# Kernel optimization log

Hardware: AMD Instinct MI355X
Metric: run time of the kernel (lower is better)

The kernel has to match this reference:

```python
import math
import jax, jax.numpy as jnp
import numpy as np

B, FEAT, H, W = 4, 256, 48, 48
NH = 8
PE = 10            # pe_dim -> 3*PE = 30 positional channels
DK = FEAT // NH    # 32
DV = FEAT // NH    # 32
SCALE = 2.0 * math.pi
TEMPERATURE = 10000.0
BN_EPS = 1e-5


def pos_en_sine(h, w, num_pos_feats=PE):
    """3-axis sine positional encoding (y, x, and a constant 'o' axis) -> [3*PE, h, w]."""
    eps = 1e-6
    ones = jnp.ones((h, w), jnp.float32)
    y_embed = jnp.cumsum(ones, axis=0)
    x_embed = jnp.cumsum(ones, axis=1)
    y_embed = y_embed / (y_embed[-1:, :] + eps) * SCALE
    x_embed = x_embed / (x_embed[:, -1:] + eps) * SCALE
    o_embed = ones * SCALE  # third axis, constant when no explicit pos is given
    dim_t = jnp.arange(num_pos_feats, dtype=jnp.float32)
    dim_t = TEMPERATURE ** (2.0 * jnp.floor(dim_t / 2.0) / num_pos_feats)

    def enc(e):  # e: [h, w] -> [h, w, PE] interleaved sin/cos
        p = e[..., None] / dim_t
        return jnp.stack([jnp.sin(p[..., 0::2]), jnp.cos(p[..., 1::2])], axis=-1).reshape(h, w, num_pos_feats)

    pe = jnp.concatenate([enc(y_embed), enc(x_embed), enc(o_embed)], axis=-1)  # [h, w, 3*PE]
    return jnp.transpose(pe, (2, 0, 1))  # [3*PE, h, w]


def conv1x1(w, x):  # w: [out_c, in_c], x: [b, in_c, h, w]
    return jnp.einsum('oc,bchw->bohw', w, x)


def setup_inputs() -> dict:
    key = jax.random.key(0)
    ks = jax.random.split(key, 16)
    s = 0.02
    return {
        'q': jax.random.normal(ks[0], (B, FEAT, H, W), jnp.float32),
        'k': jax.random.normal(ks[1], (B, FEAT, H, W), jnp.float32),
        'v': jax.random.normal(ks[2], (B, FEAT, H, W), jnp.float32),
        'wq': jax.random.normal(ks[3], (NH * DK, FEAT + 3 * PE), jnp.float32) * s,
        'wk': jax.random.normal(ks[4], (NH * DK, FEAT + 3 * PE), jnp.float32) * s,
        'wv': jax.random.normal(ks[5], (NH * DV, FEAT), jnp.float32) * s,
        'wfc': jax.random.normal(ks[6], (FEAT, NH * DV), jnp.float32) * s,
        'w1': jax.random.normal(ks[7], (FEAT, FEAT), jnp.float32) * s,
        'b1': jnp.zeros((FEAT,), jnp.float32),
        'w2': jax.random.normal(ks[8], (FEAT, FEAT), jnp.float32) * s,
        'b2': jnp.zeros((FEAT,), jnp.float32),
        'gamma': jnp.ones((FEAT,), jnp.float32),
        'beta': jnp.zeros((FEAT,), jnp.float32),
    }


def reference(q, k, v, wq, wk, wv, wfc, w1, b1, w2, b2, gamma, beta):
    b, c, h, w = q.shape
    n = h * w
    pe = pos_en_sine(h, w)                                # [3*PE, h, w]
    peb = jnp.broadcast_to(pe[None], (b,) + pe.shape)
    qc = jnp.concatenate([q, peb], axis=1)                # [b, FEAT+30, h, w]
    kc = jnp.concatenate([k, peb], axis=1)
    # multi-head softmax attention over all spatial tokens
    Q = conv1x1(wq, qc).reshape(b, NH, DK, n)             # [b, nh, dk, n]
    K = conv1x1(wk, kc).reshape(b, NH, DK, n)
    V = conv1x1(wv, v).reshape(b, NH, DV, n)
    scores = jnp.einsum('bhdn,bhdm->bhnm', Q, K) / jnp.sqrt(jnp.float32(DK))
    attn = jax.nn.softmax(scores, axis=-1)                # [b, nh, n, n]
    O = jnp.einsum('bhnm,bhdm->bhdn', attn, V).reshape(b, NH * DV, h, w)
    O = conv1x1(wfc, O)                                   # [b, FEAT, h, w]
    # pointwise FFN + residual
    h1 = jax.nn.relu(conv1x1(w1, O) + b1[None, :, None, None])
    h2 = conv1x1(w2, h1) + b2[None, :, None, None]
    out = O + h2
    # BatchNorm2d (training mode: batch statistics over (b, h, w), biased var)
    mean = jnp.mean(out, axis=(0, 2, 3), keepdims=True)
    var = jnp.var(out, axis=(0, 2, 3), keepdims=True)
    out = (out - mean) / jnp.sqrt(var + BN_EPS)
    out = out * gamma[None, :, None, None] + beta[None, :, None, None]
    return out
```

## Files before the change

### kernel.cpp

```cpp
#include <hip/hip_runtime.h>
#include <hip/hip_bf16.h>

#define NTOK 2304

typedef short  short8  __attribute__((ext_vector_type(8)));
typedef unsigned short ushort8v __attribute__((ext_vector_type(8)));
typedef float  f32x4   __attribute__((ext_vector_type(4)));

static __device__ __forceinline__ unsigned short f2bfu(float f){
  __hip_bfloat16 h = __float2bfloat16(f);
  union { __hip_bfloat16 h; unsigned short u; } cv; cv.h = h; return cv.u;
}

static __device__ __forceinline__ void plane32(unsigned &a, unsigned &b){
  asm("v_permlane32_swap_b32 %0, %1" : "+v"(a), "+v"(b));
}
static __device__ __forceinline__ void plane16(unsigned &a, unsigned &b){
  asm("v_permlane16_swap_b32 %0, %1" : "+v"(a), "+v"(b));
}
static __device__ __forceinline__ short8 xpose_p(f32x4 sa, f32x4 sb){
  unsigned x0, x1, y0, y1;
  asm("v_cvt_pk_bf16_f32 %0, %1, %2" : "=v"(x0) : "v"(sa[0]), "v"(sa[1]));
  asm("v_cvt_pk_bf16_f32 %0, %1, %2" : "=v"(x1) : "v"(sa[2]), "v"(sa[3]));
  asm("v_cvt_pk_bf16_f32 %0, %1, %2" : "=v"(y0) : "v"(sb[0]), "v"(sb[1]));
  asm("v_cvt_pk_bf16_f32 %0, %1, %2" : "=v"(y1) : "v"(sb[2]), "v"(sb[3]));
  plane32(x0, y0);
  plane32(x1, y1);
  plane16(x0, y0);
  plane16(x1, y1);
  union { unsigned u[4]; short8 s; } r;
  r.u[0] = x0; r.u[1] = x1; r.u[2] = y0; r.u[3] = y1;
  return r.s;
}


__global__ void trip_kernel(float* out, int n){
  int i = blockIdx.x*256 + threadIdx.x;
  if (i < n) out[i] = 1000.0f;
}

__global__ __launch_bounds__(256) void setup_kernel(
    const float* __restrict__ q, const float* __restrict__ k,
    const float* __restrict__ v,
    const float* __restrict__ wq, const float* __restrict__ wk,
    const float* __restrict__ wv, const float* __restrict__ wfc,
    const float* __restrict__ w1, const float* __restrict__ w2,
    unsigned short* __restrict__ qT, unsigned short* __restrict__ kT,
    unsigned short* __restrict__ vT,
    unsigned short* __restrict__ wqp, unsigned short* __restrict__ wkp,
    unsigned short* __restrict__ wvb, unsigned short* __restrict__ wfcb,
    unsigned short* __restrict__ w1b, unsigned short* __restrict__ w2b,
    float* __restrict__ bns){
  const int bid = blockIdx.x;
  const int t = threadIdx.x;
  __shared__ __align__(16) unsigned short tile[64*72];

  if (bid < 1728){
    if (bid == 0){ bns[t] = 0.f; bns[256+t] = 0.f; }
    const int x = bid % 36, rem = bid / 36;
    const int y = rem % 4, z = rem / 4;
    const int tz = z >> 2, b = z & 3;
    const float* src = (tz==0) ? q : ((tz==1) ? k : v);
    unsigned short* dst = (tz==0) ? qT : ((tz==1) ? kT : vT);
    const int W = (tz==2) ? 256 : 288;
    const int n0 = x*64, c0 = y*64;
    const int jj = t & 7, cl = t >> 3;
    #pragma unroll
    for (int p=0; p<2; p++){
      int c = c0 + 32*p + cl;
      const float* s = src + (size_t)(b*256 + c)*NTOK + n0 + 8*jj;
      float4 f0 = *(const float4*)s;
      float4 f1 = *(const float4*)(s + 4);
      unsigned short* tr = tile + 32*p + cl;
      tr[(8*jj+0)*72] = f2bfu(f0.x); tr[(8*jj+1)*72] = f2bfu(f0.y);
      tr[(8*jj+2)*72] = f2bfu(f0.z); tr[(8*jj+3)*72] = f2bfu(f0.w);
      tr[(8*jj+4)*72] = f2bfu(f1.x); tr[(8*jj+5)*72] = f2bfu(f1.y);
      tr[(8*jj+6)*72] = f2bfu(f1.z); tr[(8*jj+7)*72] = f2bfu(f1.w);
    }
    __syncthreads();
    #pragma unroll
    for (int p=0; p<2; p++){
      int nl = 32*p + cl;
      ushort8v val = *(const ushort8v*)(tile + nl*72 + 8*jj);
      *(ushort8v*)(dst + (size_t)(b*2304 + n0 + nl)*W + c0 + 8*jj) = val;
    }
  } else if (bid < 1800){
    const int id2 = bid - 1728;
    const int x = id2 % 9, yy = id2 / 9;
    const int n = x*256 + t;
    unsigned short* buf = (yy < 4) ? qT : kT;
    const int b = yy & 3;
    const int i = n / 48, j = n - 48*i;
    const float k2pi = 6.283185307179586f;
    const float f = k2pi / 48.000001f;
    float ey = (float)(i+1) * f;
    float ex = (float)(j+1) * f;
    unsigned short u[32];
    #pragma unroll
    for (int p=0; p<10; p++){
      float inv = exp2f(-2.6575424759098898f * (float)(p >> 1));
      float vy = ey*inv, vx = ex*inv, vo = k2pi*inv;
      u[p]    = f2bfu((p&1) ? cosf(vy) : sinf(vy));
      u[10+p] = f2bfu((p&1) ? cosf(vx) : sinf(vx));
      u[20+p] = f2bfu((p&1) ? cosf(vo) : sinf(vo));
    }
    u[30] = 0; u[31] = 0;
    unsigned short* dst = buf + (size_t)(b*2304 + n)*288 + 256;
    #pragma unroll
    for (int m=0; m<4; m++) *(ushort8v*)(dst + 8*m) = *(const ushort8v*)(u + 8*m);
  } else if (bid < 2376){
    const int id3 = bid - 1800;
    const int x = id3 % 288, y = id3 / 288;
    const int idx = x*256 + t;
    const float* src = y ? wk : wq;
    unsigned short* dst = y ? wkp : wqp;
    const float scale = y ? 1.f : 0.25503486f;
    int row = idx / 288, col = idx - row*288;
    dst[idx] = (col < 286) ? f2bfu(src[row*286 + col] * scale) : (unsigned short)0;
  } else {
    const int id4 = bid - 2376;
    const int x = id4 % 256, y = id4 / 256;
    const int idx = x*256 + t;
    const float* src = (y==0)?wv:((y==1)?wfc:((y==2)?w1:w2));
    unsigned short* dst = (y==0)?wvb:((y==1)?wfcb:((y==2)?w1b:w2b));
    dst[idx] = f2bfu(src[idx]);
  }
}

template<int KSTEPS>
static __device__ __forceinline__ void gemm3_core(
    const unsigned short* __restrict__ a0,
    const unsigned short* __restrict__ a1,
    const unsigned short* __restrict__ a2,
    const unsigned short* __restrict__ wrow, int wstride, f32x4 acc[3][2]){
  #pragma unroll
  for (int kk=0; kk<KSTEPS; kk++){
    short8 af0 = *(const short8*)(a0 + 32*kk);
    short8 af1 = *(const short8*)(a1 + 32*kk);
    short8 af2 = *(const short8*)(a2 + 32*kk);
    #pragma unroll
    for (int to=0; to<2; to++){
      short8 bf = *(const short8*)(wrow + (size_t)(16*to)*wstride + 32*kk);
      acc[0][to] = __builtin_amdgcn_mfma_f32_16x16x32_bf16(af0, bf, acc[0][to], 0,0,0);
      acc[1][to] = __builtin_amdgcn_mfma_f32_16x16x32_bf16(af1, bf, acc[1][to], 0,0,0);
      acc[2][to] = __builtin_amdgcn_mfma_f32_16x16x32_bf16(af2, bf, acc[2][to], 0,0,0);
    }
  }
}

static __device__ __forceinline__ void epi_tok(
    const f32x4* acc, unsigned short* __restrict__ out_tok,
    int b, int tok, int n0, int lane, int quad, int cc,
    unsigned short* __restrict__ tlw){
  #pragma unroll
  for (int to=0; to<2; to++)
    #pragma unroll
    for (int r=0; r<4; r++)
      tlw[(4*quad + r)*40 + 16*to + cc] = f2bfu(acc[to][r]);
  const int row = lane & 15, ch = lane >> 4;
  ushort8v val = *(const ushort8v*)(tlw + row*40 + 8*ch);
  *(ushort8v*)(out_tok + (size_t)(b*2304 + tok + row)*256 + n0 + 8*ch) = val;
}

static __device__ __forceinline__ void epi_chan(
    const f32x4* acc, unsigned short* __restrict__ out_chan,
    int b, int tok, int n0, int quad, int cc){
  #pragma unroll
  for (int to=0; to<2; to++){
    ushort4 pk;
    pk.x = f2bfu(acc[to][0]); pk.y = f2bfu(acc[to][1]);
    pk.z = f2bfu(acc[to][2]); pk.w = f2bfu(acc[to][3]);
    *(ushort4*)(out_chan + (size_t)(b*256 + n0 + 16*to + cc)*NTOK + tok + 4*quad) = pk;
  }
}

__global__ __launch_bounds__(256) void qkv_kernel(
    const unsigned short* __restrict__ qT, const unsigned short* __restrict__ kT,
    const unsigned short* __restrict__ vT,
    const unsigned short* __restrict__ wqp, const unsigned short* __restrict__ wkp,
    const unsigned short* __restrict__ wvb,
    unsigned short* __restrict__ Qt, unsigned short* __restrict__ Kt,
    unsigned short* __restrict__ V2){
  const int t = threadIdx.x;
  const int w = t >> 6, lane = t & 63;
  const int quad = lane >> 4, cc = lane & 15;
  const int t0 = blockIdx.x*192, n0 = blockIdx.y*32;
  const int tz = blockIdx.z >> 2, b = blockIdx.z & 3;
  const int tok = t0 + 48*w;
  __shared__ __align__(16) unsigned short tl[4*16*40];
  unsigned short* tlw = tl + w*640;

  f32x4 acc[3][2];
  #pragma unroll
  for (int f=0; f<3; f++){
    acc[f][0] = (f32x4){0.f,0.f,0.f,0.f};
    acc[f][1] = acc[f][0];
  }

  if (tz == 0){
    const unsigned short* a0 = qT + (size_t)(b*2304 + tok + cc)*288 + 8*quad;
    gemm3_core<9>(a0, a0 + (size_t)16*288, a0 + (size_t)32*288,
                  wqp + (size_t)(n0 + cc)*288 + 8*quad, 288, acc);
    epi_tok(acc[0], Qt, b, tok,      n0, lane, quad, cc, tlw);
    epi_tok(acc[1], Qt, b, tok + 16, n0, lane, quad, cc, tlw);
    epi_tok(acc[2], Qt, b, tok + 32, n0, lane, quad, cc, tlw);
  } else if (tz == 1){
    const unsigned short* a0 = kT + (size_t)(b*2304 + tok + cc)*288 + 8*quad;
    gemm3_core<9>(a0, a0 + (size_t)16*288, a0 + (size_t)32*288,
                  wkp + (size_t)(n0 + cc)*288 + 8*quad, 288, acc);
    epi_tok(acc[0], Kt, b, tok,      n0, lane, quad, cc, tlw);
    epi_tok(acc[1], Kt, b, tok + 16, n0, lane, quad, cc, tlw);
    epi_tok(acc[2], Kt, b, tok + 32, n0, lane, quad, cc, tlw);
  } else {
    const unsigned short* a0 = vT + (size_t)(b*2304 + tok + cc)*256 + 8*quad;
    gemm3_core<8>(a0, a0 + (size_t)16*256, a0 + (size_t)32*256,
                  wvb + (size_t)(n0 + cc)*256 + 8*quad, 256, acc);
    epi_chan(acc[0], V2, b, tok,      n0, quad, cc);
    epi_chan(acc[1], V2, b, tok + 16, n0, quad, cc);
    epi_chan(acc[2], V2, b, tok + 32, n0, quad, cc);
  }
}

__global__ __launch_bounds__(256) void ffn_kernel(
    const unsigned short* __restrict__ AO,
    const unsigned short* __restrict__ wfcb,
    const unsigned short* __restrict__ w1b,
    const unsigned short* __restrict__ w2b,
    const float* __restrict__ b1, const float* __restrict__ b2,
    float* __restrict__ pre_out, float* __restrict__ bns){
  const int t = threadIdx.x;
  const int w = t >> 6, lane = t & 63;
  const int quad = lane >> 4, cc = lane & 15;
  const int tok0 = blockIdx.x * 16;
  const int b = blockIdx.y;
  const int ocb = 64 * w;

  __shared__ __align__(16) unsigned short T0[16*264];
  __shared__ __align__(16) unsigned short T1[16*264];

  const unsigned short* arow = AO + (size_t)(b*2304 + tok0 + cc)*256 + 8*quad;
  f32x4 acc1[4];
  acc1[0] = (f32x4){0.f,0.f,0.f,0.f}; acc1[1]=acc1[0]; acc1[2]=acc1[0]; acc1[3]=acc1[0];
  #pragma unroll
  for (int kk=0; kk<8; kk++){
    short8 af = *(const short8*)(arow + 32*kk);
    #pragma unroll
    for (int of=0; of<4; of++){
      short8 bf = *(const short8*)(wfcb + (size_t)(ocb + 16*of + cc)*256 + 8*quad + 32*kk);
      acc1[of] = __builtin_amdgcn_mfma_f32_16x16x32_bf16(af, bf, acc1[of], 0,0,0);
    }
  }
  #pragma unroll
  for (int of=0; of<4; of++)
    #pragma unroll
    for (int r=0; r<4; r++)
      T0[(4*quad + r)*264 + ocb + 16*of + cc] = f2bfu(acc1[of][r]);
  __syncthreads();

  f32x4 acc2[4];
  acc2[0] = (f32x4){0.f,0.f,0.f,0.f}; acc2[1]=acc2[0]; acc2[2]=acc2[0]; acc2[3]=acc2[0];
  #pragma unroll
  for (int kk=0; kk<8; kk++){
    short8 af = *(const short8*)(T0 + cc*264 + 8*quad + 32*kk);
    #pragma unroll
    for (int of=0; of<4; of++){
      short8 bf = *(const short8*)(w1b + (size_t)(ocb + 16*of + cc)*256 + 8*quad + 32*kk);
      acc2[of] = __builtin_amdgcn_mfma_f32_16x16x32_bf16(af, bf, acc2[of], 0,0,0);
    }
  }
  #pragma unroll
  for (int of=0; of<4; of++){
    float bv = b1[ocb + 16*of + cc];
    #pragma unroll
    for (int r=0; r<4; r++){
      float hv = fmaxf(acc2[of][r] + bv, 0.f);
      T1[(4*quad + r)*264 + ocb + 16*of + cc] = f2bfu(hv);
    }
  }
  __syncthreads();

  f32x4 acc3[4];
  acc3[0] = (f32x4){0.f,0.f,0.f,0.f}; acc3[1]=acc3[0]; acc3[2]=acc3[0]; acc3[3]=acc3[0];
  #pragma unroll
  for (int kk=0; kk<8; kk++){
    short8 af = *(const short8*)(T1 + cc*264 + 8*quad + 32*kk);
    #pragma unroll
    for (int of=0; of<4; of++){
      short8 bf = *(const short8*)(w2b + (size_t)(ocb + 16*of + cc)*256 + 8*quad + 32*kk);
      acc3[of] = __builtin_amdgcn_mfma_f32_16x16x32_bf16(af, bf, acc3[of], 0,0,0);
    }
  }
  #pragma unroll
  for (int of=0; of<4; of++){
    const int oc = ocb + 16*of + cc;
    float bv = b2[oc];
    float p0 = acc3[of][0] + bv + acc1[of][0];
    float p1 = acc3[of][1] + bv + acc1[of][1];
    float p2 = acc3[of][2] + bv + acc1[of][2];
    float p3 = acc3[of][3] + bv + acc1[of][3];
    *(float4*)(pre_out + (size_t)(b*256 + oc)*NTOK + tok0 + 4*quad) =
        make_float4(p0, p1, p2, p3);
    float s1 = (p0+p1)+(p2+p3);
    float s2 = (p0*p0+p1*p1)+(p2*p2+p3*p3);
    s1 += __shfl_xor(s1, 16, 64); s1 += __shfl_xor(s1, 32, 64);
    s2 += __shfl_xor(s2, 16, 64); s2 += __shfl_xor(s2, 32, 64);
    if (quad == 0){
      atomicAdd(&bns[oc],       s1);
      atomicAdd(&bns[256 + oc], s2);
    }
  }
}

__global__ __launch_bounds__(256) void attn_kernel(
    const unsigned short* __restrict__ Qt, const unsigned short* __restrict__ Kt,
    const unsigned short* __restrict__ V2, unsigned short* __restrict__ AO){
  const int t = threadIdx.x;
  const int w = t >> 6, lane = t & 63;
  const int quad = lane >> 4, cc = lane & 15;
  const int h = blockIdx.y, b = blockIdx.z;
  const int q0 = blockIdx.x*48;

  const unsigned short* qb = Qt + (size_t)(b*2304 + q0 + cc)*256 + h*32 + 8*quad;
  short8 qf0 = *(const short8*)(qb);
  short8 qf1 = *(const short8*)(qb + 16*256);
  short8 qf2 = *(const short8*)(qb + 32*256);

  const unsigned short* kb = Kt + (size_t)(b*2304 + cc)*256 + h*32 + 8*quad;
  const unsigned short* vb = V2 + (size_t)(b*256 + h*32 + cc)*NTOK + 8*quad;

  __shared__ __align__(16) float mg_lds[4*1600];

  f32x4 o00={0.f,0.f,0.f,0.f}, o10=o00, o01=o00, o11=o00, o02=o00, o12=o00;
  float lsum0=0.f, lsum1=0.f, lsum2=0.f;

  const int kstart = w*576;
  short8 kf0 = *(const short8*)(kb + (size_t)kstart*256);
  short8 kf1 = *(const short8*)(kb + (size_t)(kstart+16)*256);
  short8 vf0 = *(const short8*)(vb + kstart);
  short8 vf1 = *(const short8*)(vb + (size_t)16*NTOK + kstart);

  #pragma unroll 1
  for (int it = 0; it < 18; ++it){
    const int ko = kstart + it*32;
    const int rk = (it < 17) ? ko + 32 : kstart;
    const f32x4 z = {0.f,0.f,0.f,0.f};

    f32x4 s00 = __builtin_amdgcn_mfma_f32_16x16x32_bf16(kf0, qf0, z, 0,0,0);
    f32x4 s10 = __builtin_amdgcn_mfma_f32_16x16x32_bf16(kf1, qf0, z, 0,0,0);
    f32x4 s01 = __builtin_amdgcn_mfma_f32_16x16x32_bf16(kf0, qf1, z, 0,0,0);
    f32x4 s11 = __builtin_amdgcn_mfma_f32_16x16x32_bf16(kf1, qf1, z, 0,0,0);
    f32x4 s02 = __builtin_amdgcn_mfma_f32_16x16x32_bf16(kf0, qf2, z, 0,0,0);
    f32x4 s12 = __builtin_amdgcn_mfma_f32_16x16x32_bf16(kf1, qf2, z, 0,0,0);
    kf0 = *(const short8*)(kb + (size_t)rk*256);
    kf1 = *(const short8*)(kb + (size_t)(rk+16)*256);

    #pragma unroll
    for (int r=0; r<4; r++){
      s00[r] = __builtin_amdgcn_exp2f(s00[r]);
      s10[r] = __builtin_amdgcn_exp2f(s10[r]);
      s01[r] = __builtin_amdgcn_exp2f(s01[r]);
      s11[r] = __builtin_amdgcn_exp2f(s11[r]);
      s02[r] = __builtin_amdgcn_exp2f(s02[r]);
      s12[r] = __builtin_amdgcn_exp2f(s12[r]);
    }
    lsum0 += ((s00[0]+s00[1])+(s00[2]+s00[3])) + ((s10[0]+s10[1])+(s10[2]+s10[3]));
    lsum1 += ((s01[0]+s01[1])+(s01[2]+s01[3])) + ((s11[0]+s11[1])+(s11[2]+s11[3]));
    lsum2 += ((s02[0]+s02[1])+(s02[2]+s02[3])) + ((s12[0]+s12[1])+(s12[2]+s12[3]));

    short8 pf0 = xpose_p(s00, s10);
    short8 pf1 = xpose_p(s01, s11);
    short8 pf2 = xpose_p(s02, s12);

    o00 = __builtin_amdgcn_mfma_f32_16x16x32_bf16(vf0, pf0, o00, 0,0,0);
    o10 = __builtin_amdgcn_mfma_f32_16x16x32_bf16(vf1, pf0, o10, 0,0,0);
    o01 = __builtin_amdgcn_mfma_f32_16x16x32_bf16(vf0, pf1, o01, 0,0,0);
    o11 = __builtin_amdgcn_mfma_f32_16x16x32_bf16(vf1, pf1, o11, 0,0,0);
    o02 = __builtin_amdgcn_mfma_f32_16x16x32_bf16(vf0, pf2, o02, 0,0,0);
    o12 = __builtin_amdgcn_mfma_f32_16x16x32_bf16(vf1, pf2, o12, 0,0,0);
    vf0 = *(const short8*)(vb + rk);
    vf1 = *(const short8*)(vb + (size_t)16*NTOK + rk);
  }

  lsum0 += __shfl_xor(lsum0, 16, 64); lsum0 += __shfl_xor(lsum0, 32, 64);
  lsum1 += __shfl_xor(lsum1, 16, 64); lsum1 += __shfl_xor(lsum1, 32, 64);
  lsum2 += __shfl_xor(lsum2, 16, 64); lsum2 += __shfl_xor(lsum2, 32, 64);

  float* mg = mg_lds + w*1600;
  #pragma unroll
  for (int i=0;i<4;i++){
    mg[(0*8 + 0*4 + i)*64 + lane] = o00[i];
    mg[(0*8 + 1*4 + i)*64 + lane] = o10[i];
    mg[(1*8 + 0*4 + i)*64 + lane] = o01[i];
    mg[(1*8 + 1*4 + i)*64 + lane] = o11[i];
    mg[(2*8 + 0*4 + i)*64 + lane] = o02[i];
    mg[(2*8 + 1*4 + i)*64 + lane] = o12[i];
  }
  if (quad == 0){
    mg[1536 +  0 + cc] = lsum0;
    mg[1536 + 16 + cc] = lsum1;
    mg[1536 + 32 + cc] = lsum2;
  }
  __syncthreads();

  if (w < 3){
    const float* m0 = mg_lds;
    const float* m1 = mg_lds + 1600;
    const float* m2 = mg_lds + 3200;
    const float* m3 = mg_lds + 4800;
    const int la = 1536 + w*16 + cc;
    float ls = (m0[la] + m1[la]) + (m2[la] + m3[la]);
    float inv = 1.f / ls;

    float r0, r1, r2, r3, r4, r5, r6, r7;
    {
      int a0 = (w*8 + 0)*64 + lane;
      r0 = (m0[a0] + m1[a0]) + (m2[a0] + m3[a0]);
      int a1 = (w*8 + 1)*64 + lane;
      r1 = (m0[a1] + m1[a1]) + (m2[a1] + m3[a1]);
      int a2 = (w*8 + 2)*64 + lane;
      r2 = (m0[a2] + m1[a2]) + (m2[a2] + m3[a2]);
      int a3 = (w*8 + 3)*64 + lane;
      r3 = (m0[a3] + m1[a3]) + (m2[a3] + m3[a3]);
      int a4 = (w*8 + 4)*64 + lane;
      r4 = (m0[a4] + m1[a4]) + (m2[a4] + m3[a4]);
      int a5 = (w*8 + 5)*64 + lane;
      r5 = (m0[a5] + m1[a5]) + (m2[a5] + m3[a5]);
      int a6 = (w*8 + 6)*64 + lane;
      r6 = (m0[a6] + m1[a6]) + (m2[a6] + m3[a6]);
      int a7 = (w*8 + 7)*64 + lane;
      r7 = (m0[a7] + m1[a7]) + (m2[a7] + m3[a7]);
    }

    const int qcol = q0 + w*16 + cc;
    unsigned short* dst = AO + (size_t)(b*2304 + qcol)*256 + h*32 + 4*quad;
    ushort4 p0;
    p0.x = f2bfu(r0*inv); p0.y = f2bfu(r1*inv);
    p0.z = f2bfu(r2*inv); p0.w = f2bfu(r3*inv);
    *(ushort4*)(dst) = p0;
    ushort4 p1;
    p1.x = f2bfu(r4*inv); p1.y = f2bfu(r5*inv);
    p1.z = f2bfu(r6*inv); p1.w = f2bfu(r7*inv);
    *(ushort4*)(dst + 16) = p1;
  }
}

__global__ __launch_bounds__(256) void bn_final_kernel(
    const float* __restrict__ pre, const float* __restrict__ bns,
    const float* __restrict__ g, const float* __restrict__ bt,
    float* __restrict__ out){
  int i0 = (blockIdx.x*256 + threadIdx.x)*4;
  int ch = (i0 / NTOK) & 255;
  float mean = bns[ch] * (1.f/9216.f);
  float var  = bns[256+ch] * (1.f/9216.f) - mean*mean;
  float scl = g[ch] * rsqrtf(fmaxf(var, 0.f) + 1e-5f);
  float sh  = bt[ch] - mean*scl;
  float4 x = *(const float4*)(pre + i0);
  *(float4*)(out + i0) = make_float4(x.x*scl+sh, x.y*scl+sh, x.z*scl+sh, x.w*scl+sh);
}

extern "C" void kernel_launch(void* const* d_in, const int* in_sizes, int n_in,
                              void* d_out, int out_size, void* d_ws, size_t ws_size,
                              hipStream_t stream){
  const size_t NEED = 2112 + (size_t)15155200*2;
  if (ws_size < NEED){
    trip_kernel<<<dim3((out_size+255)/256), dim3(256), 0, stream>>>((float*)d_out, out_size);
    return;
  }
  const float* q   = (const float*)d_in[0];
  const float* k   = (const float*)d_in[1];
  const float* v   = (const float*)d_in[2];
  const float* wq  = (const float*)d_in[3];
  const float* wk  = (const float*)d_in[4];
  const float* wv  = (const float*)d_in[5];
  const float* wfc = (const float*)d_in[6];
  const float* w1  = (const float*)d_in[7];
  const float* b1  = (const float*)d_in[8];
  const float* w2  = (const float*)d_in[9];
  const float* b2  = (const float*)d_in[10];
  const float* gm  = (const float*)d_in[11];
  const float* bt  = (const float*)d_in[12];

  float* ws  = (float*)d_ws;
  float* bns = ws;
  unsigned short* ub = (unsigned short*)(ws + 528);
  unsigned short* u_qT = ub;
  unsigned short* u_kT = ub + 2654208;
  unsigned short* u_vT = ub + 5308416;
  unsigned short* u_Qt = ub + 7667712;
  unsigned short* u_Kt = ub + 10027008;
  unsigned short* u_V2 = ub + 12386304;
  unsigned short* wqp  = ub + 14745600;
  unsigned short* wkp  = ub + 14819328;
  unsigned short* wvb  = ub + 14893056;
  unsigned short* wfcb = ub + 14958592;
  unsigned short* w1b  = ub + 15024128;
  unsigned short* w2b  = ub + 15089664;
  unsigned short* AO  = u_qT;
  float* pre = (float*)(u_Kt);

  setup_kernel<<<dim3(3400), dim3(256), 0, stream>>>(
      q, k, v, wq, wk, wv, wfc, w1, w2,
      u_qT, u_kT, u_vT, wqp, wkp, wvb, wfcb, w1b, w2b, bns);

  qkv_kernel<<<dim3(12,8,12), dim3(256), 0, stream>>>(u_qT, u_kT, u_vT, wqp, wkp, wvb, u_Qt, u_Kt, u_V2);

  attn_kernel<<<dim3(48,8,4), dim3(256), 0, stream>>>(u_Qt, u_Kt, u_V2, AO);

  ffn_kernel<<<dim3(144,4), dim3(256), 0, stream>>>(AO, wfcb, w1b, w2b, b1, b2, pre, bns);

  bn_final_kernel<<<dim3(2304), dim3(256), 0, stream>>>(pre, bns, gm, bt, (float*)d_out);
}
```

Before: 221.5 us.

## Remap attention blocks to XCDs per head and stagger key-chunk start order

The attention grid becomes a flat 1D launch. Each block index is decoded so that all query blocks of a given (batch, head) group land on the same XCD, where they can share that XCD's L2 copy of K and V. Each block also starts its key loop at a rotated chunk offset, so concurrent blocks do not all hit the same K/V addresses at once. The cost is some extra index arithmetic, and correctness depends on the wrap-around order still summing every key chunk, which an unnormalized softmax accumulation allows.

Result: no change. 219.9 us (-0.7%).

```diff
diff --git a/kernel.cpp b/kernel.cpp
--- a/kernel.cpp
+++ b/kernel.cpp
@@ -317,8 +317,16 @@
   const int t = threadIdx.x;
   const int w = t >> 6, lane = t & 63;
   const int quad = lane >> 4, cc = lane & 15;
-  const int h = blockIdx.y, b = blockIdx.z;
-  const int q0 = blockIdx.x*48;
+
+  const int flat = blockIdx.x;
+  const int xcd = flat & 7;
+  const int ii  = flat >> 3;
+  const int sub = ii / 48;
+  const int g   = xcd*4 + sub;
+  const int qblk = ii - sub*48;
+  const int b = g >> 3, h = g & 7;
+  const int q0 = qblk*48;
+  const int ph = qblk % 18;
 
   const unsigned short* qb = Qt + (size_t)(b*2304 + q0 + cc)*256 + h*32 + 8*quad;
   short8 qf0 = *(const short8*)(qb);
@@ -334,15 +342,19 @@
   float lsum0=0.f, lsum1=0.f, lsum2=0.f;
 
   const int kstart = w*576;
-  short8 kf0 = *(const short8*)(kb + (size_t)kstart*256);
-  short8 kf1 = *(const short8*)(kb + (size_t)(kstart+16)*256);
-  short8 vf0 = *(const short8*)(vb + kstart);
-  short8 vf1 = *(const short8*)(vb + (size_t)16*NTOK + kstart);
+  int kc = ph;
+  {
+    const int k0 = kstart + kc*32;
+  }
+  short8 kf0 = *(const short8*)(kb + (size_t)(kstart + kc*32)*256);
+  short8 kf1 = *(const short8*)(kb + (size_t)(kstart + kc*32 + 16)*256);
+  short8 vf0 = *(const short8*)(vb + kstart + kc*32);
+  short8 vf1 = *(const short8*)(vb + (size_t)16*NTOK + kstart + kc*32);
 
   #pragma unroll 1
   for (int it = 0; it < 18; ++it){
-    const int ko = kstart + it*32;
-    const int rk = (it < 17) ? ko + 32 : kstart;
+    int kn = kc + 1; if (kn == 18) kn = 0;
+    const int rk = kstart + kn*32;
     const f32x4 z = {0.f,0.f,0.f,0.f};
 
     f32x4 s00 = __builtin_amdgcn_mfma_f32_16x16x32_bf16(kf0, qf0, z, 0,0,0);
@@ -379,6 +391,8 @@
     o12 = __builtin_amdgcn_mfma_f32_16x16x32_bf16(vf1, pf2, o12, 0,0,0);
     vf0 = *(const short8*)(vb + rk);
     vf1 = *(const short8*)(vb + (size_t)16*NTOK + rk);
+
+    kc = kn;
   }
 
   lsum0 += __shfl_xor(lsum0, 16, 64); lsum0 += __shfl_xor(lsum0, 32, 64);
@@ -504,7 +518,7 @@
 
   qkv_kernel<<<dim3(12,8,12), dim3(256), 0, stream>>>(u_qT, u_kT, u_vT, wqp, wkp, wvb, u_Qt, u_Kt, u_V2);
 
-  attn_kernel<<<dim3(48,8,4), dim3(256), 0, stream>>>(u_Qt, u_Kt, u_V2, AO);
+  attn_kernel<<<dim3(1536), dim3(256), 0, stream>>>(u_Qt, u_Kt, u_V2, AO);
 
   ffn_kernel<<<dim3(144,4), dim3(256), 0, stream>>>(AO, wfcb, w1b, w2b, b1, b2, pre, bns);
 
```
